# Optimization experiments

Measured on AMD Instinct MI355X. Metric: run time of the kernel, lower is better.

Reference implementation:

```python
import jax, jax.numpy as jnp
import numpy as np

HIDDEN = 2048
INTER = 5632
B, S = 2, 2048


def _ternary(key, shape):
    # values in {-1, 0, +1}, matching 2-bit packed ternary weights
    return jax.random.randint(key, shape, -1, 2).astype(jnp.float32)


def setup_inputs() -> dict:
    key = jax.random.key(0)
    ks = jax.random.split(key, 7)
    x = jax.random.normal(ks[0], (B, S, HIDDEN), dtype=jnp.float32)
    gate_w = _ternary(ks[1], (INTER, HIDDEN))   # [intermediate, hidden]
    up_w = _ternary(ks[2], (INTER, HIDDEN))     # [intermediate, hidden]
    down_w = _ternary(ks[3], (HIDDEN, INTER))   # [hidden, intermediate]
    # per-output-channel dequant scales (positive, as from absmean quantization)
    gate_s = jax.random.uniform(ks[4], (INTER,), minval=0.01, maxval=0.1, dtype=jnp.float32)
    up_s = jax.random.uniform(ks[5], (INTER,), minval=0.01, maxval=0.1, dtype=jnp.float32)
    down_s = jax.random.uniform(ks[6], (HIDDEN,), minval=0.01, maxval=0.1, dtype=jnp.float32)
    return {"x": x, "gate_w": gate_w, "up_w": up_w, "down_w": down_w,
            "gate_s": gate_s, "up_s": up_s, "down_s": down_s}


def reference(x, gate_w, up_w, down_w, gate_s, up_s, down_s):
    # x: (B, S, H) -> flatten tokens, as in forward_hidden
    b, s, h = x.shape
    xf = x.reshape(b * s, h)
    # ternary linear = add/sub-only matmul + per-channel scale
    g = jnp.einsum('th,ih->ti', xf, gate_w) * gate_s   # (T, I)
    u = jnp.einsum('th,ih->ti', xf, up_w) * up_s       # (T, I)
    hdn = jax.nn.silu(g) * u                            # gated activation
    out = jnp.einsum('ti,hi->th', hdn, down_w) * down_s  # (T, H)
    return out.reshape(b, s, -1)
```

## Files before the change

kernel.cpp:

```cpp
#include <hip/hip_runtime.h>
#include <stdint.h>
#include <stddef.h>

#define HIDDEN 2048
#define INTER  5632
#define TOKENS 4096
#define BKD    128
#define BKI    128

typedef __attribute__((ext_vector_type(8))) _Float16 f16x8;
typedef __attribute__((ext_vector_type(4))) _Float16 f16x4;
typedef __attribute__((ext_vector_type(4))) float    f32x4;
typedef __attribute__((ext_vector_type(4))) int      i32x4;

__device__ __forceinline__ int swz8(int row, int q) {
    return row * 8 + ((q + row) & 7);
}

#define GLDS16(g, l) __builtin_amdgcn_global_load_lds( \
    (__attribute__((address_space(1))) void*)(g), \
    (__attribute__((address_space(3))) void*)(l), 16, 0, 0)

__device__ __forceinline__ int pack4i8(float4 f) {
    return ((int)(signed char)(int)f.x & 255)
         | (((int)(signed char)(int)f.y & 255) << 8)
         | (((int)(signed char)(int)f.z & 255) << 16)
         | (((int)(signed char)(int)f.w) << 24);
}

__global__ __launch_bounds__(256)
void prepass(const float* __restrict__ x,
             const float4* __restrict__ gw, const float4* __restrict__ uw,
             const float4* __restrict__ dw,
             int8_t* __restrict__ xq, float* __restrict__ xs,
             int* __restrict__ go, int* __restrict__ uo,
             _Float16* __restrict__ dno) {
    const int tid = threadIdx.x;
    if (blockIdx.x < 1024) {
        const int wave = tid >> 6;
        const int lane = tid & 63;
        const int t    = blockIdx.x * 4 + wave;
        const float4* row = (const float4*)(x + (size_t)t * HIDDEN);
        float4 v[8];
        #pragma unroll
        for (int j = 0; j < 8; ++j) v[j] = row[lane + 64 * j];
        float m = 0.0f;
        #pragma unroll
        for (int j = 0; j < 8; ++j) {
            m = fmaxf(m, fmaxf(fmaxf(fabsf(v[j].x), fabsf(v[j].y)),
                               fmaxf(fabsf(v[j].z), fabsf(v[j].w))));
        }
        #pragma unroll
        for (int off = 32; off; off >>= 1)
            m = fmaxf(m, __shfl_xor(m, off, 64));
        m = fmaxf(m, 1e-20f);
        if (lane == 0) xs[t] = m * (1.0f / 127.0f);
        const float inv = 127.0f / m;
        int* oq = (int*)(xq + (size_t)t * HIDDEN);
        #pragma unroll
        for (int j = 0; j < 8; ++j) {
            float4 f = v[j];
            f.x *= inv; f.y *= inv; f.z *= inv; f.w *= inv;
            float4 r;
            r.x = rintf(f.x); r.y = rintf(f.y); r.z = rintf(f.z); r.w = rintf(f.w);
            oq[lane + 64 * j] = pack4i8(r);
        }
        return;
    }
    const int NA = INTER * HIDDEN / 16;
    const int NC = INTER * HIDDEN / 8;
    const int stride = 2048 * 256;
    for (int u = (blockIdx.x - 1024) * 256 + tid; u < 2 * NA + NC; u += stride) {
        if (u < 2 * NA) {
            const bool is_g = u < NA;
            const int j = is_g ? u : u - NA;
            const float4* src = (is_g ? gw : uw) + (size_t)j * 4;
            float4 f0 = src[0], f1 = src[1], f2 = src[2], f3 = src[3];
            int4 p;
            p.x = pack4i8(f0); p.y = pack4i8(f1);
            p.z = pack4i8(f2); p.w = pack4i8(f3);
            ((int4*)(is_g ? go : uo))[j] = p;
        } else {
            const int j = u - 2 * NA;
            const float4* src = dw + (size_t)j * 2;
            float4 a = src[0], b = src[1];
            f16x8 o;
            o[0] = (_Float16)a.x; o[1] = (_Float16)a.y;
            o[2] = (_Float16)a.z; o[3] = (_Float16)a.w;
            o[4] = (_Float16)b.x; o[5] = (_Float16)b.y;
            o[6] = (_Float16)b.z; o[7] = (_Float16)b.w;
            *(f16x8*)(dno + (size_t)j * 8) = o;
        }
    }
}

__global__ __launch_bounds__(256, 2)
void gemm_gateup(const int8_t* __restrict__ Xq,
                 const int8_t* __restrict__ Wg,
                 const int8_t* __restrict__ Wu,
                 const float* __restrict__ xs,
                 const float* __restrict__ gs,
                 const float* __restrict__ us,
                 _Float16* __restrict__ Hm) {
    __shared__ int8_t As [128 * BKI];
    __shared__ int8_t Bgs[128 * BKI];
    __shared__ int8_t Bus[128 * BKI];

    const int pid   = (blockIdx.x % 8) * 176 + blockIdx.x / 8;
    const int local = pid % (16 * 44);
    const int bm    = ((pid / (16 * 44)) * 16 + (local & 15)) * 128;
    const int bn    = (local >> 4) * 128;

    const int tid  = threadIdx.x;
    const int lane = tid & 63;
    const int wave = tid >> 6;
    const int wm   = (wave >> 1) * 64;
    const int wn   = (wave & 1) * 64;
    const int l15  = lane & 15;
    const int lq   = lane >> 4;

    int rowA[4], sgA[4];
    #pragma unroll
    for (int j = 0; j < 4; ++j) {
        const int f = tid + 256 * j;
        rowA[j] = f >> 3;
        sgA[j]  = (((f & 7) - rowA[j]) & 7) * 16;
    }

    i32x4 accg[4][4] = {};
    i32x4 accu[4][4] = {};

    for (int k0 = 0; k0 < HIDDEN; k0 += BKI) {
        #pragma unroll
        for (int j = 0; j < 4; ++j) {
            const int f = tid + 256 * j;
            const int8_t* pX = Xq + (size_t)(bm + rowA[j]) * HIDDEN + k0 + sgA[j];
            const int8_t* pG = Wg + (size_t)(bn + rowA[j]) * HIDDEN + k0 + sgA[j];
            const int8_t* pU = Wu + (size_t)(bn + rowA[j]) * HIDDEN + k0 + sgA[j];
            GLDS16(pX, &As [f * 16]);
            GLDS16(pG, &Bgs[f * 16]);
            GLDS16(pU, &Bus[f * 16]);
        }
        __syncthreads();

        #pragma unroll
        for (int ks = 0; ks < 2; ++ks) {
            const int q = ks * 4 + lq;
            i32x4 a[4];
            #pragma unroll
            for (int im = 0; im < 4; ++im)
                a[im] = *(const i32x4*)&As[swz8(wm + im * 16 + l15, q) * 16];
            #pragma unroll
            for (int jn = 0; jn < 4; ++jn) {
                i32x4 bg = *(const i32x4*)&Bgs[swz8(wn + jn * 16 + l15, q) * 16];
                i32x4 bu = *(const i32x4*)&Bus[swz8(wn + jn * 16 + l15, q) * 16];
                #pragma unroll
                for (int im = 0; im < 4; ++im) {
                    accg[im][jn] = __builtin_amdgcn_mfma_i32_16x16x64_i8(a[im], bg, accg[im][jn], 0, 0, 0);
                    accu[im][jn] = __builtin_amdgcn_mfma_i32_16x16x64_i8(a[im], bu, accu[im][jn], 0, 0, 0);
                }
            }
        }
        __syncthreads();
    }

    #pragma unroll
    for (int jn = 0; jn < 4; ++jn) {
        const int col = bn + wn + jn * 16 + l15;
        const float sg = gs[col];
        const float su = us[col];
        #pragma unroll
        for (int im = 0; im < 4; ++im) {
            const int rbase = bm + wm + im * 16 + lq * 4;
            #pragma unroll
            for (int r = 0; r < 4; ++r) {
                const int row = rbase + r;
                const float st = xs[row];
                float g = (float)accg[im][jn][r] * st * sg;
                float u = (float)accu[im][jn][r] * st * su;
                float h = (g / (1.0f + __expf(-g))) * u;
                Hm[(size_t)row * INTER + col] = (_Float16)h;
            }
        }
    }
}

__global__ __launch_bounds__(256, 2)
void gemm_down(const _Float16* __restrict__ Hm,
               const _Float16* __restrict__ Wd,
               const float* __restrict__ dsc,
               float* __restrict__ out) {
    __shared__ _Float16 As0[128 * 64];
    __shared__ _Float16 As1[128 * 64];
    __shared__ _Float16 Bs0[128 * 64];
    __shared__ _Float16 Bs1[128 * 64];

    const int pid = (blockIdx.x % 8) * 64 + blockIdx.x / 8;
    const int loc = pid & 255;
    const int bm  = ((pid >> 8) * 16 + (loc & 15)) * 128;
    const int bn  = (loc >> 4) * 128;

    const int tid  = threadIdx.x;
    const int lane = tid & 63;
    const int wave = tid >> 6;
    const int wm   = (wave >> 1) * 64;
    const int wn   = (wave & 1) * 64;
    const int l15  = lane & 15;
    const int lq   = lane >> 4;

    int rS[4], sS[4];
    #pragma unroll
    for (int j = 0; j < 4; ++j) {
        const int f = tid + 256 * j;
        rS[j] = f >> 3;
        sS[j] = (((f & 7) - (f >> 3)) & 7) * 8;
    }

    const _Float16* gA = Hm + (size_t)bm * INTER;
    const _Float16* gB = Wd + (size_t)bn * INTER;

    f32x4 acc[4][4] = {};

    for (int k0 = 0; k0 < INTER; k0 += BKD) {
        #pragma unroll
        for (int j = 0; j < 4; ++j) {
            const int f = tid + 256 * j;
            const size_t oA = (size_t)rS[j] * INTER + k0 + sS[j];
            GLDS16(gA + oA,      &As0[f * 8]);
            GLDS16(gA + oA + 64, &As1[f * 8]);
            GLDS16(gB + oA,      &Bs0[f * 8]);
            GLDS16(gB + oA + 64, &Bs1[f * 8]);
        }
        __syncthreads();

        #pragma unroll
        for (int ks = 0; ks < 4; ++ks) {
            const _Float16* A_ = (ks < 2) ? As0 : As1;
            const _Float16* B_ = (ks < 2) ? Bs0 : Bs1;
            const int q = (ks & 1) * 4 + lq;
            f16x8 a[4];
            #pragma unroll
            for (int im = 0; im < 4; ++im)
                a[im] = *(const f16x8*)&A_[swz8(wm + im * 16 + l15, q) * 8];
            #pragma unroll
            for (int jn = 0; jn < 4; ++jn) {
                f16x8 b = *(const f16x8*)&B_[swz8(wn + jn * 16 + l15, q) * 8];
                #pragma unroll
                for (int im = 0; im < 4; ++im)
                    acc[im][jn] = __builtin_amdgcn_mfma_f32_16x16x32_f16(a[im], b, acc[im][jn], 0, 0, 0);
            }
        }
        __syncthreads();
    }

    #pragma unroll
    for (int jn = 0; jn < 4; ++jn) {
        const int col = bn + wn + jn * 16 + l15;
        const float sd = dsc[col];
        #pragma unroll
        for (int im = 0; im < 4; ++im) {
            const int rbase = bm + wm + im * 16 + lq * 4;
            #pragma unroll
            for (int r = 0; r < 4; ++r)
                out[(size_t)(rbase + r) * HIDDEN + col] = acc[im][jn][r] * sd;
        }
    }
}

extern "C" void kernel_launch(void* const* d_in, const int* in_sizes, int n_in,
                              void* d_out, int out_size, void* d_ws, size_t ws_size,
                              hipStream_t stream) {
    const float* x   = (const float*)d_in[0];
    const float* gw  = (const float*)d_in[1];
    const float* uw  = (const float*)d_in[2];
    const float* dw  = (const float*)d_in[3];
    const float* gsc = (const float*)d_in[4];
    const float* usc = (const float*)d_in[5];
    const float* dsc = (const float*)d_in[6];
    float* out = (float*)d_out;

    char* ws = (char*)d_ws;
    int8_t*   Xq  = (int8_t*)(ws);
    int8_t*   Wg8 = (int8_t*)(ws + 8388608ull);
    int8_t*   Wu8 = (int8_t*)(ws + 19922944ull);
    _Float16* Wdh = (_Float16*)(ws + 31457280ull);
    _Float16* Hm  = (_Float16*)(ws + 54525952ull);
    float*    xs  = (float*)(ws + 100663296ull);

    prepass<<<1024 + 2048, 256, 0, stream>>>(
        x, (const float4*)gw, (const float4*)uw, (const float4*)dw,
        Xq, xs, (int*)Wg8, (int*)Wu8, Wdh);

    gemm_gateup<<<(INTER / 128) * (TOKENS / 128), 256, 0, stream>>>(
        Xq, Wg8, Wu8, xs, gsc, usc, Hm);
    gemm_down<<<(HIDDEN / 128) * (TOKENS / 128), 256, 0, stream>>>(
        Hm, Wdh, dsc, out);
}
```

Measured before the change: 371.2 us.

## Prefetch next K tile into LDS while computing from registers

Both GEMM loops now read each LDS tile fully into registers, synchronize, then issue the global-to-LDS loads for the next K tile before running the MFMAs. The goal is to overlap global memory latency with matrix math, using one LDS buffer and register staging instead of double buffering. In exchange, each thread holds many more live fragment registers (for example 32 f16x8 in the down projection), which may lower occupancy or cause spills.

```diff
diff --git a/kernel.cpp b/kernel.cpp
--- a/kernel.cpp
+++ b/kernel.cpp
@@ -7,6 +7,8 @@
 #define TOKENS 4096
 #define BKD    128
 #define BKI    128
+#define NT_GU  (HIDDEN / BKI)
+#define NT_DN  (INTER / BKD)
 
 typedef __attribute__((ext_vector_type(8))) _Float16 f16x8;
 typedef __attribute__((ext_vector_type(4))) _Float16 f16x4;
@@ -127,42 +129,53 @@
         sgA[j]  = (((f & 7) - rowA[j]) & 7) * 16;
     }
 
+    #define STG_GU(k0) do { \
+        _Pragma("unroll") \
+        for (int j = 0; j < 4; ++j) { \
+            const int f_ = tid + 256 * j; \
+            const int8_t* pX = Xq + (size_t)(bm + rowA[j]) * HIDDEN + (k0) + sgA[j]; \
+            const int8_t* pG = Wg + (size_t)(bn + rowA[j]) * HIDDEN + (k0) + sgA[j]; \
+            const int8_t* pU = Wu + (size_t)(bn + rowA[j]) * HIDDEN + (k0) + sgA[j]; \
+            GLDS16(pX, &As [f_ * 16]); \
+            GLDS16(pG, &Bgs[f_ * 16]); \
+            GLDS16(pU, &Bus[f_ * 16]); \
+        } \
+    } while (0)
+
     i32x4 accg[4][4] = {};
     i32x4 accu[4][4] = {};
 
-    for (int k0 = 0; k0 < HIDDEN; k0 += BKI) {
-        #pragma unroll
-        for (int j = 0; j < 4; ++j) {
-            const int f = tid + 256 * j;
-            const int8_t* pX = Xq + (size_t)(bm + rowA[j]) * HIDDEN + k0 + sgA[j];
-            const int8_t* pG = Wg + (size_t)(bn + rowA[j]) * HIDDEN + k0 + sgA[j];
-            const int8_t* pU = Wu + (size_t)(bn + rowA[j]) * HIDDEN + k0 + sgA[j];
-            GLDS16(pX, &As [f * 16]);
-            GLDS16(pG, &Bgs[f * 16]);
-            GLDS16(pU, &Bus[f * 16]);
-        }
-        __syncthreads();
-
+    STG_GU(0);
+    __syncthreads();
+
+    for (int t = 0; t < NT_GU; ++t) {
+        i32x4 a[2][4], bg[2][4], bu[2][4];
         #pragma unroll
         for (int ks = 0; ks < 2; ++ks) {
             const int q = ks * 4 + lq;
-            i32x4 a[4];
             #pragma unroll
             for (int im = 0; im < 4; ++im)
-                a[im] = *(const i32x4*)&As[swz8(wm + im * 16 + l15, q) * 16];
+                a[ks][im] = *(const i32x4*)&As[swz8(wm + im * 16 + l15, q) * 16];
             #pragma unroll
             for (int jn = 0; jn < 4; ++jn) {
-                i32x4 bg = *(const i32x4*)&Bgs[swz8(wn + jn * 16 + l15, q) * 16];
-                i32x4 bu = *(const i32x4*)&Bus[swz8(wn + jn * 16 + l15, q) * 16];
+                bg[ks][jn] = *(const i32x4*)&Bgs[swz8(wn + jn * 16 + l15, q) * 16];
+                bu[ks][jn] = *(const i32x4*)&Bus[swz8(wn + jn * 16 + l15, q) * 16];
+            }
+        }
+        __syncthreads();
+        if (t + 1 < NT_GU) STG_GU((t + 1) * BKI);
+        #pragma unroll
+        for (int ks = 0; ks < 2; ++ks)
+            #pragma unroll
+            for (int jn = 0; jn < 4; ++jn)
                 #pragma unroll
                 for (int im = 0; im < 4; ++im) {
-                    accg[im][jn] = __builtin_amdgcn_mfma_i32_16x16x64_i8(a[im], bg, accg[im][jn], 0, 0, 0);
-                    accu[im][jn] = __builtin_amdgcn_mfma_i32_16x16x64_i8(a[im], bu, accu[im][jn], 0, 0, 0);
+                    accg[im][jn] = __builtin_amdgcn_mfma_i32_16x16x64_i8(a[ks][im], bg[ks][jn], accg[im][jn], 0, 0, 0);
+                    accu[im][jn] = __builtin_amdgcn_mfma_i32_16x16x64_i8(a[ks][im], bu[ks][jn], accu[im][jn], 0, 0, 0);
                 }
-            }
-        }
         __syncthreads();
     }
+    #undef STG_GU
 
     #pragma unroll
     for (int jn = 0; jn < 4; ++jn) {
@@ -219,39 +232,49 @@
     const _Float16* gA = Hm + (size_t)bm * INTER;
     const _Float16* gB = Wd + (size_t)bn * INTER;
 
+    #define STG_DN(k0) do { \
+        _Pragma("unroll") \
+        for (int j = 0; j < 4; ++j) { \
+            const int f_ = tid + 256 * j; \
+            const size_t o_ = (size_t)rS[j] * INTER + (k0) + sS[j]; \
+            GLDS16(gA + o_,      &As0[f_ * 8]); \
+            GLDS16(gA + o_ + 64, &As1[f_ * 8]); \
+            GLDS16(gB + o_,      &Bs0[f_ * 8]); \
+            GLDS16(gB + o_ + 64, &Bs1[f_ * 8]); \
+        } \
+    } while (0)
+
     f32x4 acc[4][4] = {};
 
-    for (int k0 = 0; k0 < INTER; k0 += BKD) {
-        #pragma unroll
-        for (int j = 0; j < 4; ++j) {
-            const int f = tid + 256 * j;
-            const size_t oA = (size_t)rS[j] * INTER + k0 + sS[j];
-            GLDS16(gA + oA,      &As0[f * 8]);
-            GLDS16(gA + oA + 64, &As1[f * 8]);
-            GLDS16(gB + oA,      &Bs0[f * 8]);
-            GLDS16(gB + oA + 64, &Bs1[f * 8]);
-        }
-        __syncthreads();
-
+    STG_DN(0);
+    __syncthreads();
+
+    for (int t = 0; t < NT_DN; ++t) {
+        f16x8 a[4][4], b[4][4];
         #pragma unroll
         for (int ks = 0; ks < 4; ++ks) {
             const _Float16* A_ = (ks < 2) ? As0 : As1;
             const _Float16* B_ = (ks < 2) ? Bs0 : Bs1;
             const int q = (ks & 1) * 4 + lq;
-            f16x8 a[4];
             #pragma unroll
             for (int im = 0; im < 4; ++im)
-                a[im] = *(const f16x8*)&A_[swz8(wm + im * 16 + l15, q) * 8];
-            #pragma unroll
-            for (int jn = 0; jn < 4; ++jn) {
-                f16x8 b = *(const f16x8*)&B_[swz8(wn + jn * 16 + l15, q) * 8];
+                a[ks][im] = *(const f16x8*)&A_[swz8(wm + im * 16 + l15, q) * 8];
+            #pragma unroll
+            for (int jn = 0; jn < 4; ++jn)
+                b[ks][jn] = *(const f16x8*)&B_[swz8(wn + jn * 16 + l15, q) * 8];
+        }
+        __syncthreads();
+        if (t + 1 < NT_DN) STG_DN((t + 1) * BKD);
+        #pragma unroll
+        for (int ks = 0; ks < 4; ++ks)
+            #pragma unroll
+            for (int jn = 0; jn < 4; ++jn)
                 #pragma unroll
                 for (int im = 0; im < 4; ++im)
-                    acc[im][jn] = __builtin_amdgcn_mfma_f32_16x16x32_f16(a[im], b, acc[im][jn], 0, 0, 0);
-            }
-        }
+                    acc[im][jn] = __builtin_amdgcn_mfma_f32_16x16x32_f16(a[ks][im], b[ks][jn], acc[im][jn], 0, 0, 0);
         __syncthreads();
     }
+    #undef STG_DN
 
     #pragma unroll
     for (int jn = 0; jn < 4; ++jn) {
```

After: 362.8 us. -2.3%, faster.
